# Optimization experiments

Hardware: AMD Instinct MI355X
Metric: run time of the kernel (lower is better)

## Reference

```python
import jax, jax.numpy as jnp
import numpy as np

B, OBS, DH, N, DK, DV, TASKS, OUT = 4096, 512, 1024, 8, 256, 1024, 10, 128
LOG_SIG_MIN, LOG_SIG_MAX = -20.0, 2.0


def _lin(k, fan_in, shape):
    return jax.random.normal(k, shape, jnp.float32) / np.sqrt(fan_in)


def setup_inputs() -> dict:
    ks = jax.random.split(jax.random.key(0), 18)
    return {
        "x": jax.random.normal(ks[0], (B, OBS), jnp.float32),
        "task_id": 3,
        # base MLP (2 layers)
        "Wb1": _lin(ks[1], OBS, (OBS, DH)), "bb1": jnp.zeros((DH,), jnp.float32),
        "Wb2": _lin(ks[2], DH, (DH, DH)), "bb2": jnp.zeros((DH,), jnp.float32),
        # per-expert MLPs (stacked over expert dim n)
        "We1": _lin(ks[3], DH, (N, DH, DH)), "be1": jnp.zeros((N, DH), jnp.float32),
        "We2": _lin(ks[4], DH, (N, DH, DH)), "be2": jnp.zeros((N, DH), jnp.float32),
        # per-expert attention v / k heads
        "Wv": _lin(ks[5], DH, (N, DH, DV)), "bv": jnp.zeros((N, DV), jnp.float32),
        "Wk": _lin(ks[6], DH, (N, DH, DK)), "bk": jnp.zeros((N, DK), jnp.float32),
        # per-task q networks (input = one-hot task vector of size TASKS)
        "Wq": _lin(ks[7], TASKS, (TASKS, TASKS, DK)), "bq": jnp.zeros((TASKS, DK), jnp.float32),
        # tower + last
        "Wt1": _lin(ks[8], DV, (DV, DH)), "bt1": jnp.zeros((DH,), jnp.float32),
        "Wl": _lin(ks[9], DH, (DH, OUT)) * 0.003, "bl": jnp.zeros((OUT,), jnp.float32),
    }


def reference(x, task_id, Wb1, bb1, Wb2, bb2, We1, be1, We2, be2,
              Wv, bv, Wk, bk, Wq, bq, Wt1, bt1, Wl, bl):
    act = jax.nn.relu
    # base: [B, DH]
    h = act(act(x @ Wb1 + bb1) @ Wb2 + bb2)
    # all experts at once: e [N, B, DH]
    e = act(jnp.einsum('bd,ndh->nbh', h, We1) + be1[:, None, :])
    e = act(jnp.einsum('nbd,ndh->nbh', e, We2) + be2[:, None, :])
    # attention values / keys per expert
    v = jnp.einsum('nbd,ndv->nbv', e, Wv) + bv[:, None, :]   # [N, B, DV]
    k = jnp.einsum('nbd,ndk->nbk', e, Wk) + bk[:, None, :]   # [N, B, DK]
    # q from one-hot task index through task-specific q net
    task_idx = jax.nn.one_hot(task_id, TASKS, dtype=x.dtype)  # [TASKS]
    q = task_idx @ Wq[task_id] + bq[task_id]                  # [DK]
    # raw (unnormalized) weights, as in the original (alphas are computed but unused)
    expkq = jnp.einsum('nbk,k->nb', k, q)                     # [N, B]
    res = jnp.einsum('nbv,nb->bv', v, expkq)                  # [B, DV]
    t = act(res @ Wt1 + bt1)
    out = t @ Wl + bl                                          # [B, OUT]
    mean, log_std = jnp.split(out, 2, axis=-1)
    log_std = jnp.clip(log_std, LOG_SIG_MIN, LOG_SIG_MAX)
    std = jnp.exp(log_std)
    return mean, std, log_std
```

## Files before the change

kernel.cpp:

```cpp
#include <hip/hip_runtime.h>
#include <hip/hip_bf16.h>

typedef unsigned short u16;
typedef unsigned int   u32;
typedef __attribute__((ext_vector_type(4))) float  f32x4;
typedef __attribute__((ext_vector_type(8))) __bf16 bf16x8;

#define B_    4096
#define OBS_  512
#define DH_   1024
#define NEXP_ 8
#define DK_   256
#define DV_   1024

__device__ __forceinline__ float b2f(u32 lo16) {
  return __builtin_bit_cast(float, lo16 << 16);
}
__device__ __forceinline__ u16 f2b(float f) {
  u32 u = __builtin_bit_cast(u32, f);
  return (u16)((u + 0x7fffu + ((u >> 16) & 1u)) >> 16);
}
__device__ __forceinline__ void gl_lds16(const u16* g, u16* l) {
  __builtin_amdgcn_global_load_lds(
      (__attribute__((address_space(1))) void*)(void*)g,
      (__attribute__((address_space(3))) void*)(void*)l,
      16, 0, 0);
}

__device__ __forceinline__ void tconv_body(const float* __restrict__ in,
                                           u16* __restrict__ outp,
                                           int R, int C, int rem, int tid) {
  __shared__ float tile[32][33];
  int gxs = (C == 128) ? 2 : 5;
  int c0 = (rem & ((1 << gxs) - 1)) * 32;
  int r0 = (rem >> gxs) * 32;
  int tx = tid & 31, ty = tid >> 5;
#pragma unroll
  for (int i = 0; i < 4; ++i)
    tile[ty + i * 8][tx] = in[(long)(r0 + ty + i * 8) * C + c0 + tx];
  __syncthreads();
#pragma unroll
  for (int i = 0; i < 4; ++i)
    outp[(long)(c0 + ty + i * 8) * R + r0 + tx] = f2b(tile[tx][ty + i * 8]);
}

__global__ __launch_bounds__(256)
void prep(const float* __restrict__ x,  u16* __restrict__ xb,
          const float* __restrict__ Wb1, u16* __restrict__ Wb1T,
          const float* __restrict__ Wb2, u16* __restrict__ Wb2T,
          const float* __restrict__ We1, u16* __restrict__ We1T,
          const float* __restrict__ We2, u16* __restrict__ We2T,
          const float* __restrict__ Wv,  u16* __restrict__ WvT,
          const float* __restrict__ Wt1, u16* __restrict__ Wt1T,
          const float* __restrict__ Wl,  u16* __restrict__ WlT) {
  int tid = threadIdx.x;
  int bid = blockIdx.x;
  if (bid < 2048) {
    long i = ((long)bid * 256 + tid) * 4;
    float4 v = *(const float4*)(x + i);
    u16 o[4] = { f2b(v.x), f2b(v.y), f2b(v.z), f2b(v.w) };
    *(uint2*)(xb + i) = *(const uint2*)o;
    return;
  }
  bid -= 2048;
  if (bid < 512)  { tconv_body(Wb1, Wb1T, 512, 1024, bid, tid); return; }
  bid -= 512;
  if (bid < 1024) { tconv_body(Wb2, Wb2T, 1024, 1024, bid, tid); return; }
  bid -= 1024;
  if (bid < 8192) {
    int z = bid >> 10, rem = bid & 1023;
    tconv_body(We1 + (long)z * DH_ * DH_, We1T + (long)z * DH_ * DH_, 1024, 1024, rem, tid);
    return;
  }
  bid -= 8192;
  if (bid < 8192) {
    int z = bid >> 10, rem = bid & 1023;
    tconv_body(We2 + (long)z * DH_ * DH_, We2T + (long)z * DH_ * DH_, 1024, 1024, rem, tid);
    return;
  }
  bid -= 8192;
  if (bid < 8192) { tconv_body(Wv, WvT, 8192, 1024, bid, tid); return; }
  bid -= 8192;
  if (bid < 1024) { tconv_body(Wt1, Wt1T, 1024, 1024, bid, tid); return; }
  bid -= 1024;
  tconv_body(Wl, WlT, 1024, 128, bid, tid);
}

__global__ __launch_bounds__(256)
void wnq_cn(const float* __restrict__ Wq, const float* __restrict__ bq,
            const float* __restrict__ bk, const int* __restrict__ task,
            const float* __restrict__ Wk, float* __restrict__ wnq,
            float* __restrict__ cn) {
  int t = *task;
  const float* qrow = Wq + (long)(t * 10 + t) * DK_;
  const float* brow = bq + (long)t * DK_;
  int lane = threadIdx.x & 63;
  int bid = blockIdx.x;
  if (bid < 2048) {
    int row = bid * 4 + (threadIdx.x >> 6);
    const float* wr = Wk + (long)row * DK_;
    float s = 0.f;
#pragma unroll
    for (int i = 0; i < 4; ++i) {
      int j = lane + i * 64;
      s += wr[j] * (qrow[j] + brow[j]);
    }
    for (int off = 32; off; off >>= 1) s += __shfl_xor(s, off);
    if (lane == 0) wnq[row] = s;
  } else {
    int w = threadIdx.x >> 6;
    for (int n = w; n < NEXP_; n += 4) {
      float s = 0.f;
#pragma unroll
      for (int i = 0; i < 4; ++i) {
        int j = lane + i * 64;
        s += bk[n * DK_ + j] * (qrow[j] + brow[j]);
      }
      for (int off = 32; off; off >>= 1) s += __shfl_xor(s, off);
      if (lane == 0) cn[n] = s;
    }
  }
}

__global__ __launch_bounds__(256)
void expkq_k(const u16* __restrict__ e2, const float* __restrict__ wnq,
             const float* __restrict__ cn, float* __restrict__ ekq) {
  int row  = blockIdx.x * 4 + (threadIdx.x >> 6);
  int n    = row >> 12;
  int lane = threadIdx.x & 63;
  const u16*   er = e2 + (long)row * DH_ + lane * 16;
  const float* w  = wnq + n * DH_ + lane * 16;
  uint4 p0 = *(const uint4*)er;
  uint4 p1 = *(const uint4*)(er + 8);
  float s = 0.f;
  const u32* a = (const u32*)&p0;
  const u32* c = (const u32*)&p1;
#pragma unroll
  for (int i = 0; i < 4; ++i) {
    float2 w0 = *(const float2*)(w + 2 * i);
    float2 w1 = *(const float2*)(w + 8 + 2 * i);
    s += b2f(a[i] & 0xffffu) * w0.x + b2f(a[i] >> 16) * w0.y;
    s += b2f(c[i] & 0xffffu) * w1.x + b2f(c[i] >> 16) * w1.y;
  }
  for (int off = 32; off; off >>= 1) s += __shfl_xor(s, off);
  if (lane == 0) ekq[row] = s + cn[n];
}

template<int RELU, int OUT, int LDA, int LDB>
__global__ __launch_bounds__(256, 4)
void gemm_bt(const u16* __restrict__ A, const u16* __restrict__ Bt,
             const float* __restrict__ bias, void* __restrict__ Cv,
             int M, int N, int kper, int ksplit,
             long aB, long bB, long biasB, long cB) {
  const int zz = blockIdx.z;
  const int split = zz % ksplit;
  const int batch = zz / ksplit;
  A  += (long)batch * aB + (long)split * kper;
  Bt += (long)batch * bB + (long)split * kper;

  int m_idx = blockIdx.y, n_idx = blockIdx.x;
  if (gridDim.x == 8) {
    int f = blockIdx.x + (blockIdx.y << 3);
    int xcd = f & 7, j = f >> 3;
    n_idx = j & 7;
    m_idx = (xcd << 2) | (j >> 3);
  }
  const int m0 = m_idx * 128, n0 = n_idx * 128;

  __shared__ u16 As[128 * 64];
  __shared__ u16 Bs[128 * 64];
  const int tid  = threadIdx.x;
  const int lane = tid & 63, wid = tid >> 6;
  const int wm = (wid >> 1) * 64, wn = (wid & 1) * 64;
  const int lr = lane & 15, quad = lane >> 4;
  const int srow = lane >> 3;
  const int scol = ((lane & 7) ^ srow) * 8;

  const u16* ap0 = A  + (long)(m0 + wid * 32 +  0 + srow) * LDA + scol;
  const u16* ap1 = A  + (long)(m0 + wid * 32 +  8 + srow) * LDA + scol;
  const u16* ap2 = A  + (long)(m0 + wid * 32 + 16 + srow) * LDA + scol;
  const u16* ap3 = A  + (long)(m0 + wid * 32 + 24 + srow) * LDA + scol;
  const u16* bp0 = Bt + (long)(n0 + wid * 32 +  0 + srow) * LDB + scol;
  const u16* bp1 = Bt + (long)(n0 + wid * 32 +  8 + srow) * LDB + scol;
  const u16* bp2 = Bt + (long)(n0 + wid * 32 + 16 + srow) * LDB + scol;
  const u16* bp3 = Bt + (long)(n0 + wid * 32 + 24 + srow) * LDB + scol;
  u16* la = &As[wid * 2048];
  u16* lb = &Bs[wid * 2048];

  const int rsw = lr & 7;
  const int aB0 = (wm + lr) * 64 + ((quad    ) ^ rsw) * 8;
  const int aB1 = (wm + lr) * 64 + ((quad + 4) ^ rsw) * 8;
  const int bB0 = (wn + lr) * 64 + ((quad    ) ^ rsw) * 8;
  const int bB1 = (wn + lr) * 64 + ((quad + 4) ^ rsw) * 8;

  f32x4 acc[4][4] = {};

  for (int k0 = 0; k0 < kper; k0 += 64) {
    __syncthreads();
    gl_lds16(ap0 + k0, la);        gl_lds16(ap1 + k0, la + 512);
    gl_lds16(ap2 + k0, la + 1024); gl_lds16(ap3 + k0, la + 1536);
    gl_lds16(bp0 + k0, lb);        gl_lds16(bp1 + k0, lb + 512);
    gl_lds16(bp2 + k0, lb + 1024); gl_lds16(bp3 + k0, lb + 1536);
    __syncthreads();
#pragma unroll
    for (int h = 0; h < 2; ++h) {
      const int ab = h ? aB1 : aB0, bb = h ? bB1 : bB0;
      bf16x8 af[4], bfr[4];
#pragma unroll
      for (int i = 0; i < 4; ++i) af[i]  = *(const bf16x8*)(&As[ab + i * 1024]);
#pragma unroll
      for (int i = 0; i < 4; ++i) bfr[i] = *(const bf16x8*)(&Bs[bb + i * 1024]);
#pragma unroll
      for (int mi = 0; mi < 4; ++mi)
#pragma unroll
        for (int ni = 0; ni < 4; ++ni)
          acc[mi][ni] = __builtin_amdgcn_mfma_f32_16x16x32_bf16(af[mi], bfr[ni], acc[mi][ni], 0, 0, 0);
    }
  }

  if (OUT == 1) {
    float* C = (float*)Cv + (long)split * ((long)M * N);
#pragma unroll
    for (int mi = 0; mi < 4; ++mi)
#pragma unroll
      for (int ni = 0; ni < 4; ++ni) {
        int col = n0 + wn + ni * 16 + lr;
#pragma unroll
        for (int r = 0; r < 4; ++r) {
          int row = m0 + wm + mi * 16 + quad * 4 + r;
          C[(long)row * N + col] = acc[mi][ni][r];
        }
      }
  } else {
    u16* C = (u16*)Cv + (long)batch * cB;
    const float* bptr = bias ? bias + (long)batch * biasB : nullptr;
#pragma unroll
    for (int mi = 0; mi < 4; ++mi)
#pragma unroll
      for (int ni = 0; ni < 4; ++ni) {
        int col = n0 + wn + ni * 16 + lr;
        float bcol = bptr ? bptr[col] : 0.f;
#pragma unroll
        for (int r = 0; r < 4; ++r) {
          int row = m0 + wm + mi * 16 + quad * 4 + r;
          float v = acc[mi][ni][r] + bcol;
          if (RELU) v = fmaxf(v, 0.f);
          C[(long)row * N + col] = f2b(v);
        }
      }
  }
}

__global__ __launch_bounds__(256)
void reduce2_relu(const float* __restrict__ part, const float* __restrict__ bias,
                  u16* __restrict__ outp, int N, long stride) {
  long f4 = ((long)blockIdx.x * 256 + threadIdx.x) * 4;
  float4 v0 = *(const float4*)(part + f4);
  float4 v1 = *(const float4*)(part + stride + f4);
  int col = (int)(f4 % N);
  float4 bb = *(const float4*)(bias + col);
  u16 o[4];
  o[0] = f2b(fmaxf(v0.x + v1.x + bb.x, 0.f));
  o[1] = f2b(fmaxf(v0.y + v1.y + bb.y, 0.f));
  o[2] = f2b(fmaxf(v0.z + v1.z + bb.z, 0.f));
  o[3] = f2b(fmaxf(v0.w + v1.w + bb.w, 0.f));
  *(uint2*)(outp + f4) = *(const uint2*)o;
}

__global__ __launch_bounds__(256)
void reduce_res(const u16* __restrict__ y, const float* __restrict__ ekq,
                const float* __restrict__ bvp, u16* __restrict__ res) {
  long f8 = ((long)blockIdx.x * 256 + threadIdx.x) * 8;
  int b = (int)(f8 >> 10);
  int v = (int)(f8 & (DV_ - 1));
  float acc[8] = {};
#pragma unroll
  for (int n = 0; n < NEXP_; ++n) {
    float s = ekq[n * B_ + b];
    uint4 p = *(const uint4*)(y + ((long)(n * B_ + b) * DV_) + v);
    const u32* pi = (const u32*)&p;
    float4 b0 = *(const float4*)(bvp + n * DV_ + v);
    float4 b1 = *(const float4*)(bvp + n * DV_ + v + 4);
    acc[0] += s * (b2f(pi[0] & 0xffffu) + b0.x);
    acc[1] += s * (b2f(pi[0] >> 16)     + b0.y);
    acc[2] += s * (b2f(pi[1] & 0xffffu) + b0.z);
    acc[3] += s * (b2f(pi[1] >> 16)     + b0.w);
    acc[4] += s * (b2f(pi[2] & 0xffffu) + b1.x);
    acc[5] += s * (b2f(pi[2] >> 16)     + b1.y);
    acc[6] += s * (b2f(pi[3] & 0xffffu) + b1.z);
    acc[7] += s * (b2f(pi[3] >> 16)     + b1.w);
  }
  u16 o[8];
#pragma unroll
  for (int i = 0; i < 8; ++i) o[i] = f2b(acc[i]);
  *(uint4*)(res + f8) = *(const uint4*)o;
}

__global__ __launch_bounds__(256)
void reduce_final(const float* __restrict__ part, const float* __restrict__ bl,
                  float* __restrict__ outp) {
  int flat = blockIdx.x * 256 + threadIdx.x;
  int c = flat & 127, b = flat >> 7;
  float v = bl[c];
  const long S = (long)B_ * 128;
#pragma unroll
  for (int s = 0; s < 8; ++s) v += part[s * S + flat];
  if (c < 64) {
    outp[b * 64 + c] = v;
  } else {
    int i = b * 64 + (c - 64);
    float ls = fminf(fmaxf(v, -20.f), 2.f);
    outp[262144 + i] = expf(ls);
    outp[524288 + i] = ls;
  }
}

extern "C" void kernel_launch(void* const* d_in, const int* in_sizes, int n_in,
                              void* d_out, int out_size, void* d_ws, size_t ws_size,
                              hipStream_t stream) {
  const float* x   = (const float*)d_in[0];
  const int*   task= (const int*)  d_in[1];
  const float* Wb1 = (const float*)d_in[2];
  const float* bb1 = (const float*)d_in[3];
  const float* Wb2 = (const float*)d_in[4];
  const float* bb2 = (const float*)d_in[5];
  const float* We1 = (const float*)d_in[6];
  const float* be1 = (const float*)d_in[7];
  const float* We2 = (const float*)d_in[8];
  const float* be2 = (const float*)d_in[9];
  const float* Wv  = (const float*)d_in[10];
  const float* bv  = (const float*)d_in[11];
  const float* Wk  = (const float*)d_in[12];
  const float* bk  = (const float*)d_in[13];
  const float* Wq  = (const float*)d_in[14];
  const float* bq  = (const float*)d_in[15];
  const float* Wt1 = (const float*)d_in[16];
  const float* bt1 = (const float*)d_in[17];
  const float* Wl  = (const float*)d_in[18];
  const float* bl  = (const float*)d_in[19];
  float* outp = (float*)d_out;

  char* ws = (char*)d_ws;
  size_t off = 0;
  auto alloc = [&](size_t bytes) -> char* {
    char* p = ws + off;
    off += (bytes + 255) & ~(size_t)255;
    return p;
  };

  u16* xb    = (u16*)alloc((size_t)B_ * OBS_ * 2);
  u16* Wb1T  = (u16*)alloc((size_t)DH_ * OBS_ * 2);
  u16* Wb2T  = (u16*)alloc((size_t)DH_ * DH_ * 2);
  u16* We1T  = (u16*)alloc((size_t)NEXP_ * DH_ * DH_ * 2);
  u16* We2T  = (u16*)alloc((size_t)NEXP_ * DH_ * DH_ * 2);
  u16* WvT   = (u16*)alloc((size_t)DV_ * NEXP_ * DH_ * 2);
  u16* Wt1T  = (u16*)alloc((size_t)DH_ * DV_ * 2);
  u16* WlT   = (u16*)alloc((size_t)128 * DH_ * 2);
  u16* h1    = (u16*)alloc((size_t)B_ * DH_ * 2);
  u16* h     = (u16*)alloc((size_t)B_ * DH_ * 2);
  u16* e1    = (u16*)alloc((size_t)NEXP_ * B_ * DH_ * 2);
  u16* e2    = (u16*)alloc((size_t)NEXP_ * B_ * DH_ * 2);
  float* cn  = (float*)alloc(NEXP_ * 4);
  float* wnq = (float*)alloc((size_t)NEXP_ * DH_ * 4);
  float* ekq = (float*)alloc((size_t)NEXP_ * B_ * 4);
  float* partA = (float*)e1;
  u16*   y     = e1;
  u16*   res   = h1;
  u16*   tt    = h;
  float* partB = (float*)e2;

  prep<<<29312, 256, 0, stream>>>(x, xb, Wb1, Wb1T, Wb2, Wb2T, We1, We1T,
                                  We2, We2T, Wv, WvT, Wt1, Wt1T, Wl, WlT);
  wnq_cn<<<2049, 256, 0, stream>>>(Wq, bq, bk, task, Wk, wnq, cn);

  const long S1 = (long)B_ * DH_;
  gemm_bt<0, 1, OBS_, OBS_><<<dim3(8, 32, 2), 256, 0, stream>>>(xb, Wb1T, nullptr, partA,
      B_, DH_, 256, 2, 0, 0, 0, 0);
  reduce2_relu<<<4096, 256, 0, stream>>>(partA, bb1, h1, DH_, S1);
  gemm_bt<0, 1, DH_, DH_><<<dim3(8, 32, 2), 256, 0, stream>>>(h1, Wb2T, nullptr, partA,
      B_, DH_, 512, 2, 0, 0, 0, 0);
  reduce2_relu<<<4096, 256, 0, stream>>>(partA, bb2, h, DH_, S1);
  gemm_bt<1, 0, DH_, DH_><<<dim3(8, 32, 8), 256, 0, stream>>>(h, We1T, be1, e1,
      B_, DH_, DH_, 1, 0, (long)DH_ * DH_, DH_, (long)B_ * DH_);
  gemm_bt<1, 0, DH_, DH_><<<dim3(8, 32, 8), 256, 0, stream>>>(e1, We2T, be2, e2,
      B_, DH_, DH_, 1, (long)B_ * DH_, (long)DH_ * DH_, DH_, (long)B_ * DH_);
  expkq_k<<<(NEXP_ * B_) / 4, 256, 0, stream>>>(e2, wnq, cn, ekq);
  gemm_bt<0, 0, DH_, NEXP_ * DH_><<<dim3(8, 32, 8), 256, 0, stream>>>(e2, WvT, nullptr, y,
      B_, DV_, DH_, 1, (long)B_ * DH_, DH_, 0, (long)B_ * DV_);
  reduce_res<<<2048, 256, 0, stream>>>(y, ekq, bv, res);
  gemm_bt<0, 1, DV_, DV_><<<dim3(8, 32, 2), 256, 0, stream>>>(res, Wt1T, nullptr, partB,
      B_, DH_, 512, 2, 0, 0, 0, 0);
  reduce2_relu<<<4096, 256, 0, stream>>>(partB, bt1, tt, DH_, S1);
  gemm_bt<0, 1, DH_, DH_><<<dim3(1, 32, 8), 256, 0, stream>>>(tt, WlT, nullptr, partB,
      B_, 128, 128, 8, 0, 0, 0, 0);
  reduce_final<<<(B_ * 128) / 256, 256, 0, stream>>>(partB, bl, outp);
}
```

Baseline: 493.0 us.

## Fuse expkq into expert GEMM epilogue, add 256x128 GEMM tile, merge prep kernels

Adds gemm_bt2, a 512-thread GEMM with 256x128 tiles, and uses it for the three large batched expert GEMMs. The second expert GEMM now computes the key-query dot product in its epilogue with a lane shuffle reduction and atomicAdd into ekq, which removes the separate expkq kernel and its full re-read of e2. The wnq/cn computation moves into the prep kernel to save a launch, and cn is added later in reduce_res. A memset is needed to zero ekq, and the float atomics make the summation order nondeterministic.

```diff
diff --git a/kernel.cpp b/kernel.cpp
--- a/kernel.cpp
+++ b/kernel.cpp
@@ -52,7 +52,11 @@
           const float* __restrict__ We2, u16* __restrict__ We2T,
           const float* __restrict__ Wv,  u16* __restrict__ WvT,
           const float* __restrict__ Wt1, u16* __restrict__ Wt1T,
-          const float* __restrict__ Wl,  u16* __restrict__ WlT) {
+          const float* __restrict__ Wl,  u16* __restrict__ WlT,
+          const float* __restrict__ Wq,  const float* __restrict__ bq,
+          const float* __restrict__ bk,  const int* __restrict__ task,
+          const float* __restrict__ Wk,  float* __restrict__ wnq,
+          float* __restrict__ cn) {
   int tid = threadIdx.x;
   int bid = blockIdx.x;
   if (bid < 2048) {
@@ -83,21 +87,14 @@
   bid -= 8192;
   if (bid < 1024) { tconv_body(Wt1, Wt1T, 1024, 1024, bid, tid); return; }
   bid -= 1024;
-  tconv_body(Wl, WlT, 1024, 128, bid, tid);
-}
-
-__global__ __launch_bounds__(256)
-void wnq_cn(const float* __restrict__ Wq, const float* __restrict__ bq,
-            const float* __restrict__ bk, const int* __restrict__ task,
-            const float* __restrict__ Wk, float* __restrict__ wnq,
-            float* __restrict__ cn) {
+  if (bid < 128)  { tconv_body(Wl, WlT, 1024, 128, bid, tid); return; }
+  bid -= 128;
   int t = *task;
   const float* qrow = Wq + (long)(t * 10 + t) * DK_;
   const float* brow = bq + (long)t * DK_;
-  int lane = threadIdx.x & 63;
-  int bid = blockIdx.x;
+  int lane = tid & 63;
   if (bid < 2048) {
-    int row = bid * 4 + (threadIdx.x >> 6);
+    int row = bid * 4 + (tid >> 6);
     const float* wr = Wk + (long)row * DK_;
     float s = 0.f;
 #pragma unroll
@@ -108,7 +105,7 @@
     for (int off = 32; off; off >>= 1) s += __shfl_xor(s, off);
     if (lane == 0) wnq[row] = s;
   } else {
-    int w = threadIdx.x >> 6;
+    int w = tid >> 6;
     for (int n = w; n < NEXP_; n += 4) {
       float s = 0.f;
 #pragma unroll
@@ -120,30 +117,6 @@
       if (lane == 0) cn[n] = s;
     }
   }
-}
-
-__global__ __launch_bounds__(256)
-void expkq_k(const u16* __restrict__ e2, const float* __restrict__ wnq,
-             const float* __restrict__ cn, float* __restrict__ ekq) {
-  int row  = blockIdx.x * 4 + (threadIdx.x >> 6);
-  int n    = row >> 12;
-  int lane = threadIdx.x & 63;
-  const u16*   er = e2 + (long)row * DH_ + lane * 16;
-  const float* w  = wnq + n * DH_ + lane * 16;
-  uint4 p0 = *(const uint4*)er;
-  uint4 p1 = *(const uint4*)(er + 8);
-  float s = 0.f;
-  const u32* a = (const u32*)&p0;
-  const u32* c = (const u32*)&p1;
-#pragma unroll
-  for (int i = 0; i < 4; ++i) {
-    float2 w0 = *(const float2*)(w + 2 * i);
-    float2 w1 = *(const float2*)(w + 8 + 2 * i);
-    s += b2f(a[i] & 0xffffu) * w0.x + b2f(a[i] >> 16) * w0.y;
-    s += b2f(c[i] & 0xffffu) * w1.x + b2f(c[i] >> 16) * w1.y;
-  }
-  for (int off = 32; off; off >>= 1) s += __shfl_xor(s, off);
-  if (lane == 0) ekq[row] = s + cn[n];
 }
 
 template<int RELU, int OUT, int LDA, int LDB>
@@ -248,6 +221,103 @@
           C[(long)row * N + col] = f2b(v);
         }
       }
+  }
+}
+
+template<int RELU, int EKQ, int LDA, int LDB>
+__global__ __launch_bounds__(512, 4)
+void gemm_bt2(const u16* __restrict__ A, const u16* __restrict__ Bt,
+              const float* __restrict__ bias, void* __restrict__ Cv,
+              int M, int N, int kper,
+              long aB, long bB, long biasB, long cB,
+              const float* __restrict__ wnq, float* __restrict__ ekqOut) {
+  const int batch = blockIdx.z;
+  A  += (long)batch * aB;
+  Bt += (long)batch * bB;
+
+  int f = blockIdx.x + (blockIdx.y << 3);
+  int xcd = f & 7, j = f >> 3;
+  const int n_idx = j & 7;
+  const int m_idx = (xcd << 1) | (j >> 3);
+  const int m0 = m_idx * 256, n0 = n_idx * 128;
+
+  __shared__ u16 As[256 * 64];
+  __shared__ u16 Bs[128 * 64];
+  const int tid  = threadIdx.x;
+  const int lane = tid & 63, wid = tid >> 6;
+  const int wm = (wid >> 1) * 64, wn = (wid & 1) * 64;
+  const int lr = lane & 15, quad = lane >> 4;
+  const int srow = lane >> 3;
+  const int scol = ((lane & 7) ^ srow) * 8;
+
+  const u16* ap0 = A  + (long)(m0 + wid * 32 +  0 + srow) * LDA + scol;
+  const u16* ap1 = A  + (long)(m0 + wid * 32 +  8 + srow) * LDA + scol;
+  const u16* ap2 = A  + (long)(m0 + wid * 32 + 16 + srow) * LDA + scol;
+  const u16* ap3 = A  + (long)(m0 + wid * 32 + 24 + srow) * LDA + scol;
+  const u16* bp0 = Bt + (long)(n0 + wid * 16 +  0 + srow) * LDB + scol;
+  const u16* bp1 = Bt + (long)(n0 + wid * 16 +  8 + srow) * LDB + scol;
+  u16* la = &As[wid * 2048];
+  u16* lb = &Bs[wid * 1024];
+
+  const int rsw = lr & 7;
+  const int aB0 = (wm + lr) * 64 + ((quad    ) ^ rsw) * 8;
+  const int aB1 = (wm + lr) * 64 + ((quad + 4) ^ rsw) * 8;
+  const int bB0 = (wn + lr) * 64 + ((quad    ) ^ rsw) * 8;
+  const int bB1 = (wn + lr) * 64 + ((quad + 4) ^ rsw) * 8;
+
+  f32x4 acc[4][4] = {};
+
+  for (int k0 = 0; k0 < kper; k0 += 64) {
+    __syncthreads();
+    gl_lds16(ap0 + k0, la);        gl_lds16(ap1 + k0, la + 512);
+    gl_lds16(ap2 + k0, la + 1024); gl_lds16(ap3 + k0, la + 1536);
+    gl_lds16(bp0 + k0, lb);        gl_lds16(bp1 + k0, lb + 512);
+    __syncthreads();
+#pragma unroll
+    for (int h = 0; h < 2; ++h) {
+      const int ab = h ? aB1 : aB0, bb = h ? bB1 : bB0;
+      bf16x8 af[4], bfr[4];
+#pragma unroll
+      for (int i = 0; i < 4; ++i) af[i]  = *(const bf16x8*)(&As[ab + i * 1024]);
+#pragma unroll
+      for (int i = 0; i < 4; ++i) bfr[i] = *(const bf16x8*)(&Bs[bb + i * 1024]);
+#pragma unroll
+      for (int mi = 0; mi < 4; ++mi)
+#pragma unroll
+        for (int ni = 0; ni < 4; ++ni)
+          acc[mi][ni] = __builtin_amdgcn_mfma_f32_16x16x32_bf16(af[mi], bfr[ni], acc[mi][ni], 0, 0, 0);
+    }
+  }
+
+  u16* C = (u16*)Cv + (long)batch * cB;
+  const float* bptr = bias ? bias + (long)batch * biasB : nullptr;
+#pragma unroll
+  for (int mi = 0; mi < 4; ++mi) {
+    float psum[4] = {0.f, 0.f, 0.f, 0.f};
+#pragma unroll
+    for (int ni = 0; ni < 4; ++ni) {
+      int col = n0 + wn + ni * 16 + lr;
+      float bcol = bptr ? bptr[col] : 0.f;
+      float wq = EKQ ? wnq[(long)batch * N + col] : 0.f;
+#pragma unroll
+      for (int r = 0; r < 4; ++r) {
+        int row = m0 + wm + mi * 16 + quad * 4 + r;
+        float v = acc[mi][ni][r] + bcol;
+        if (RELU) v = fmaxf(v, 0.f);
+        C[(long)row * N + col] = f2b(v);
+        if (EKQ) psum[r] += v * wq;
+      }
+    }
+    if (EKQ) {
+#pragma unroll
+      for (int r = 0; r < 4; ++r) {
+        float s = psum[r];
+        s += __shfl_xor(s, 1); s += __shfl_xor(s, 2);
+        s += __shfl_xor(s, 4); s += __shfl_xor(s, 8);
+        if (lr == 0)
+          atomicAdd(ekqOut + (long)batch * M + (m0 + wm + mi * 16 + quad * 4 + r), s);
+      }
+    }
   }
 }
 
@@ -269,14 +339,15 @@
 
 __global__ __launch_bounds__(256)
 void reduce_res(const u16* __restrict__ y, const float* __restrict__ ekq,
-                const float* __restrict__ bvp, u16* __restrict__ res) {
+                const float* __restrict__ cn, const float* __restrict__ bvp,
+                u16* __restrict__ res) {
   long f8 = ((long)blockIdx.x * 256 + threadIdx.x) * 8;
   int b = (int)(f8 >> 10);
   int v = (int)(f8 & (DV_ - 1));
   float acc[8] = {};
 #pragma unroll
   for (int n = 0; n < NEXP_; ++n) {
-    float s = ekq[n * B_ + b];
+    float s = ekq[n * B_ + b] + cn[n];
     uint4 p = *(const uint4*)(y + ((long)(n * B_ + b) * DV_) + v);
     const u32* pi = (const u32*)&p;
     float4 b0 = *(const float4*)(bvp + n * DV_ + v);
@@ -369,9 +440,10 @@
   u16*   tt    = h;
   float* partB = (float*)e2;
 
-  prep<<<29312, 256, 0, stream>>>(x, xb, Wb1, Wb1T, Wb2, Wb2T, We1, We1T,
-                                  We2, We2T, Wv, WvT, Wt1, Wt1T, Wl, WlT);
-  wnq_cn<<<2049, 256, 0, stream>>>(Wq, bq, bk, task, Wk, wnq, cn);
+  hipMemsetAsync(ekq, 0, (size_t)NEXP_ * B_ * 4, stream);
+  prep<<<31361, 256, 0, stream>>>(x, xb, Wb1, Wb1T, Wb2, Wb2T, We1, We1T,
+                                  We2, We2T, Wv, WvT, Wt1, Wt1T, Wl, WlT,
+                                  Wq, bq, bk, task, Wk, wnq, cn);
 
   const long S1 = (long)B_ * DH_;
   gemm_bt<0, 1, OBS_, OBS_><<<dim3(8, 32, 2), 256, 0, stream>>>(xb, Wb1T, nullptr, partA,
@@ -380,14 +452,13 @@
   gemm_bt<0, 1, DH_, DH_><<<dim3(8, 32, 2), 256, 0, stream>>>(h1, Wb2T, nullptr, partA,
       B_, DH_, 512, 2, 0, 0, 0, 0);
   reduce2_relu<<<4096, 256, 0, stream>>>(partA, bb2, h, DH_, S1);
-  gemm_bt<1, 0, DH_, DH_><<<dim3(8, 32, 8), 256, 0, stream>>>(h, We1T, be1, e1,
-      B_, DH_, DH_, 1, 0, (long)DH_ * DH_, DH_, (long)B_ * DH_);
-  gemm_bt<1, 0, DH_, DH_><<<dim3(8, 32, 8), 256, 0, stream>>>(e1, We2T, be2, e2,
-      B_, DH_, DH_, 1, (long)B_ * DH_, (long)DH_ * DH_, DH_, (long)B_ * DH_);
-  expkq_k<<<(NEXP_ * B_) / 4, 256, 0, stream>>>(e2, wnq, cn, ekq);
-  gemm_bt<0, 0, DH_, NEXP_ * DH_><<<dim3(8, 32, 8), 256, 0, stream>>>(e2, WvT, nullptr, y,
-      B_, DV_, DH_, 1, (long)B_ * DH_, DH_, 0, (long)B_ * DV_);
-  reduce_res<<<2048, 256, 0, stream>>>(y, ekq, bv, res);
+  gemm_bt2<1, 0, DH_, DH_><<<dim3(8, 16, 8), 512, 0, stream>>>(h, We1T, be1, e1,
+      B_, DH_, DH_, 0, (long)DH_ * DH_, DH_, (long)B_ * DH_, nullptr, nullptr);
+  gemm_bt2<1, 1, DH_, DH_><<<dim3(8, 16, 8), 512, 0, stream>>>(e1, We2T, be2, e2,
+      B_, DH_, DH_, (long)B_ * DH_, (long)DH_ * DH_, DH_, (long)B_ * DH_, wnq, ekq);
+  gemm_bt2<0, 0, DH_, NEXP_ * DH_><<<dim3(8, 16, 8), 512, 0, stream>>>(e2, WvT, nullptr, y,
+      B_, DV_, DH_, (long)B_ * DH_, DH_, 0, (long)B_ * DV_, nullptr, nullptr);
+  reduce_res<<<2048, 256, 0, stream>>>(y, ekq, cn, bv, res);
   gemm_bt<0, 1, DV_, DV_><<<dim3(8, 32, 2), 256, 0, stream>>>(res, Wt1T, nullptr, partB,
       B_, DH_, 512, 2, 0, 0, 0, 0);
   reduce2_relu<<<4096, 256, 0, stream>>>(partB, bt1, tt, DH_, S1);
```

Result: no change. 490.2 us (-0.6%).

## Fuse expkq dot product into expert GEMM epilogue and merge wnq into prep

Applied to the files above, without the earlier changes.

The separate expkq kernel, which re-read the whole e2 tensor, is removed. The second expert GEMM epilogue now multiplies each fp32 output by wnq, reduces across lanes with shuffles and atomically adds into a zeroed ekq buffer. The cn bias is added later in reduce_res. The wnq/cn kernel is also folded into the prep launch as extra blocks, and a memset is added. This saves a 64MB read and a launch, at the cost of epilogue work, atomics and a change in summation order (fp32 values instead of bf16-rounded ones).

```diff
diff --git a/kernel.cpp b/kernel.cpp
--- a/kernel.cpp
+++ b/kernel.cpp
@@ -52,7 +52,11 @@
           const float* __restrict__ We2, u16* __restrict__ We2T,
           const float* __restrict__ Wv,  u16* __restrict__ WvT,
           const float* __restrict__ Wt1, u16* __restrict__ Wt1T,
-          const float* __restrict__ Wl,  u16* __restrict__ WlT) {
+          const float* __restrict__ Wl,  u16* __restrict__ WlT,
+          const float* __restrict__ Wq,  const float* __restrict__ bq,
+          const float* __restrict__ bk,  const int* __restrict__ task,
+          const float* __restrict__ Wk,  float* __restrict__ wnq,
+          float* __restrict__ cn) {
   int tid = threadIdx.x;
   int bid = blockIdx.x;
   if (bid < 2048) {
@@ -83,21 +87,14 @@
   bid -= 8192;
   if (bid < 1024) { tconv_body(Wt1, Wt1T, 1024, 1024, bid, tid); return; }
   bid -= 1024;
-  tconv_body(Wl, WlT, 1024, 128, bid, tid);
-}
-
-__global__ __launch_bounds__(256)
-void wnq_cn(const float* __restrict__ Wq, const float* __restrict__ bq,
-            const float* __restrict__ bk, const int* __restrict__ task,
-            const float* __restrict__ Wk, float* __restrict__ wnq,
-            float* __restrict__ cn) {
+  if (bid < 128)  { tconv_body(Wl, WlT, 1024, 128, bid, tid); return; }
+  bid -= 128;
   int t = *task;
   const float* qrow = Wq + (long)(t * 10 + t) * DK_;
   const float* brow = bq + (long)t * DK_;
-  int lane = threadIdx.x & 63;
-  int bid = blockIdx.x;
+  int lane = tid & 63;
   if (bid < 2048) {
-    int row = bid * 4 + (threadIdx.x >> 6);
+    int row = bid * 4 + (tid >> 6);
     const float* wr = Wk + (long)row * DK_;
     float s = 0.f;
 #pragma unroll
@@ -108,7 +105,7 @@
     for (int off = 32; off; off >>= 1) s += __shfl_xor(s, off);
     if (lane == 0) wnq[row] = s;
   } else {
-    int w = threadIdx.x >> 6;
+    int w = tid >> 6;
     for (int n = w; n < NEXP_; n += 4) {
       float s = 0.f;
 #pragma unroll
@@ -122,36 +119,13 @@
   }
 }
 
-__global__ __launch_bounds__(256)
-void expkq_k(const u16* __restrict__ e2, const float* __restrict__ wnq,
-             const float* __restrict__ cn, float* __restrict__ ekq) {
-  int row  = blockIdx.x * 4 + (threadIdx.x >> 6);
-  int n    = row >> 12;
-  int lane = threadIdx.x & 63;
-  const u16*   er = e2 + (long)row * DH_ + lane * 16;
-  const float* w  = wnq + n * DH_ + lane * 16;
-  uint4 p0 = *(const uint4*)er;
-  uint4 p1 = *(const uint4*)(er + 8);
-  float s = 0.f;
-  const u32* a = (const u32*)&p0;
-  const u32* c = (const u32*)&p1;
-#pragma unroll
-  for (int i = 0; i < 4; ++i) {
-    float2 w0 = *(const float2*)(w + 2 * i);
-    float2 w1 = *(const float2*)(w + 8 + 2 * i);
-    s += b2f(a[i] & 0xffffu) * w0.x + b2f(a[i] >> 16) * w0.y;
-    s += b2f(c[i] & 0xffffu) * w1.x + b2f(c[i] >> 16) * w1.y;
-  }
-  for (int off = 32; off; off >>= 1) s += __shfl_xor(s, off);
-  if (lane == 0) ekq[row] = s + cn[n];
-}
-
-template<int RELU, int OUT, int LDA, int LDB>
+template<int RELU, int OUT, int EKQ, int LDA, int LDB>
 __global__ __launch_bounds__(256, 4)
 void gemm_bt(const u16* __restrict__ A, const u16* __restrict__ Bt,
              const float* __restrict__ bias, void* __restrict__ Cv,
              int M, int N, int kper, int ksplit,
-             long aB, long bB, long biasB, long cB) {
+             long aB, long bB, long biasB, long cB,
+             const float* __restrict__ wnq, float* __restrict__ ekqOut) {
   const int zz = blockIdx.z;
   const int split = zz % ksplit;
   const int batch = zz / ksplit;
@@ -235,19 +209,33 @@
     u16* C = (u16*)Cv + (long)batch * cB;
     const float* bptr = bias ? bias + (long)batch * biasB : nullptr;
 #pragma unroll
-    for (int mi = 0; mi < 4; ++mi)
+    for (int mi = 0; mi < 4; ++mi) {
+      float psum[4] = {0.f, 0.f, 0.f, 0.f};
 #pragma unroll
       for (int ni = 0; ni < 4; ++ni) {
         int col = n0 + wn + ni * 16 + lr;
         float bcol = bptr ? bptr[col] : 0.f;
+        float wq = EKQ ? wnq[(long)batch * N + col] : 0.f;
 #pragma unroll
         for (int r = 0; r < 4; ++r) {
           int row = m0 + wm + mi * 16 + quad * 4 + r;
           float v = acc[mi][ni][r] + bcol;
           if (RELU) v = fmaxf(v, 0.f);
           C[(long)row * N + col] = f2b(v);
+          if (EKQ) psum[r] += v * wq;
         }
       }
+      if (EKQ) {
+#pragma unroll
+        for (int r = 0; r < 4; ++r) {
+          float s = psum[r];
+          s += __shfl_xor(s, 1); s += __shfl_xor(s, 2);
+          s += __shfl_xor(s, 4); s += __shfl_xor(s, 8);
+          if (lr == 0)
+            atomicAdd(ekqOut + (long)batch * M + (m0 + wm + mi * 16 + quad * 4 + r), s);
+        }
+      }
+    }
   }
 }
 
@@ -269,14 +257,15 @@
 
 __global__ __launch_bounds__(256)
 void reduce_res(const u16* __restrict__ y, const float* __restrict__ ekq,
-                const float* __restrict__ bvp, u16* __restrict__ res) {
+                const float* __restrict__ cn, const float* __restrict__ bvp,
+                u16* __restrict__ res) {
   long f8 = ((long)blockIdx.x * 256 + threadIdx.x) * 8;
   int b = (int)(f8 >> 10);
   int v = (int)(f8 & (DV_ - 1));
   float acc[8] = {};
 #pragma unroll
   for (int n = 0; n < NEXP_; ++n) {
-    float s = ekq[n * B_ + b];
+    float s = ekq[n * B_ + b] + cn[n];
     uint4 p = *(const uint4*)(y + ((long)(n * B_ + b) * DV_) + v);
     const u32* pi = (const u32*)&p;
     float4 b0 = *(const float4*)(bvp + n * DV_ + v);
@@ -369,29 +358,29 @@
   u16*   tt    = h;
   float* partB = (float*)e2;
 
-  prep<<<29312, 256, 0, stream>>>(x, xb, Wb1, Wb1T, Wb2, Wb2T, We1, We1T,
-                                  We2, We2T, Wv, WvT, Wt1, Wt1T, Wl, WlT);
-  wnq_cn<<<2049, 256, 0, stream>>>(Wq, bq, bk, task, Wk, wnq, cn);
+  hipMemsetAsync(ekq, 0, (size_t)NEXP_ * B_ * 4, stream);
+  prep<<<31361, 256, 0, stream>>>(x, xb, Wb1, Wb1T, Wb2, Wb2T, We1, We1T,
+                                  We2, We2T, Wv, WvT, Wt1, Wt1T, Wl, WlT,
+                                  Wq, bq, bk, task, Wk, wnq, cn);
 
   const long S1 = (long)B_ * DH_;
-  gemm_bt<0, 1, OBS_, OBS_><<<dim3(8, 32, 2), 256, 0, stream>>>(xb, Wb1T, nullptr, partA,
-      B_, DH_, 256, 2, 0, 0, 0, 0);
+  gemm_bt<0, 1, 0, OBS_, OBS_><<<dim3(8, 32, 2), 256, 0, stream>>>(xb, Wb1T, nullptr, partA,
+      B_, DH_, 256, 2, 0, 0, 0, 0, nullptr, nullptr);
   reduce2_relu<<<4096, 256, 0, stream>>>(partA, bb1, h1, DH_, S1);
-  gemm_bt<0, 1, DH_, DH_><<<dim3(8, 32, 2), 256, 0, stream>>>(h1, Wb2T, nullptr, partA,
-      B_, DH_, 512, 2, 0, 0, 0, 0);
+  gemm_bt<0, 1, 0, DH_, DH_><<<dim3(8, 32, 2), 256, 0, stream>>>(h1, Wb2T, nullptr, partA,
+      B_, DH_, 512, 2, 0, 0, 0, 0, nullptr, nullptr);
   reduce2_relu<<<4096, 256, 0, stream>>>(partA, bb2, h, DH_, S1);
-  gemm_bt<1, 0, DH_, DH_><<<dim3(8, 32, 8), 256, 0, stream>>>(h, We1T, be1, e1,
-      B_, DH_, DH_, 1, 0, (long)DH_ * DH_, DH_, (long)B_ * DH_);
-  gemm_bt<1, 0, DH_, DH_><<<dim3(8, 32, 8), 256, 0, stream>>>(e1, We2T, be2, e2,
-      B_, DH_, DH_, 1, (long)B_ * DH_, (long)DH_ * DH_, DH_, (long)B_ * DH_);
-  expkq_k<<<(NEXP_ * B_) / 4, 256, 0, stream>>>(e2, wnq, cn, ekq);
-  gemm_bt<0, 0, DH_, NEXP_ * DH_><<<dim3(8, 32, 8), 256, 0, stream>>>(e2, WvT, nullptr, y,
-      B_, DV_, DH_, 1, (long)B_ * DH_, DH_, 0, (long)B_ * DV_);
-  reduce_res<<<2048, 256, 0, stream>>>(y, ekq, bv, res);
-  gemm_bt<0, 1, DV_, DV_><<<dim3(8, 32, 2), 256, 0, stream>>>(res, Wt1T, nullptr, partB,
-      B_, DH_, 512, 2, 0, 0, 0, 0);
+  gemm_bt<1, 0, 0, DH_, DH_><<<dim3(8, 32, 8), 256, 0, stream>>>(h, We1T, be1, e1,
+      B_, DH_, DH_, 1, 0, (long)DH_ * DH_, DH_, (long)B_ * DH_, nullptr, nullptr);
+  gemm_bt<1, 0, 1, DH_, DH_><<<dim3(8, 32, 8), 256, 0, stream>>>(e1, We2T, be2, e2,
+      B_, DH_, DH_, 1, (long)B_ * DH_, (long)DH_ * DH_, DH_, (long)B_ * DH_, wnq, ekq);
+  gemm_bt<0, 0, 0, DH_, NEXP_ * DH_><<<dim3(8, 32, 8), 256, 0, stream>>>(e2, WvT, nullptr, y,
+      B_, DV_, DH_, 1, (long)B_ * DH_, DH_, 0, (long)B_ * DV_, nullptr, nullptr);
+  reduce_res<<<2048, 256, 0, stream>>>(y, ekq, cn, bv, res);
+  gemm_bt<0, 1, 0, DV_, DV_><<<dim3(8, 32, 2), 256, 0, stream>>>(res, Wt1T, nullptr, partB,
+      B_, DH_, 512, 2, 0, 0, 0, 0, nullptr, nullptr);
   reduce2_relu<<<4096, 256, 0, stream>>>(partB, bt1, tt, DH_, S1);
-  gemm_bt<0, 1, DH_, DH_><<<dim3(1, 32, 8), 256, 0, stream>>>(tt, WlT, nullptr, partB,
-      B_, 128, 128, 8, 0, 0, 0, 0);
+  gemm_bt<0, 1, 0, DH_, DH_><<<dim3(1, 32, 8), 256, 0, stream>>>(tt, WlT, nullptr, partB,
+      B_, 128, 128, 8, 0, 0, 0, 0, nullptr, nullptr);
   reduce_final<<<(B_ * 128) / 256, 256, 0, stream>>>(partB, bl, outp);
 }
```

After: 494.4 us. Within noise of the previous version (+0.3%).
